# Performance work log

Hardware: AMD Instinct MI355X
Metric: run time of the kernel (lower is better)

The kernel has to match this reference:

```python
import jax, jax.numpy as jnp
import numpy as np

B = 32          # batch size
N = 32          # image dim -> P = N*N points per sample
P = N * N
F = 64          # point feature dim (= MLP output)
K = 32          # max_neighbors
R = 0.1         # ball-query radius
EPS = 1e-5      # batchnorm eps


def setup_inputs() -> dict:
    key = jax.random.key(0)
    ks = jax.random.split(key, 4)
    NP = B * P
    x = jax.random.normal(ks[0], (NP, F), jnp.float32)
    pos = jax.random.uniform(ks[1], (NP, 2), jnp.float32)
    # module requires exactly N*N points per sample, sorted by batch
    batch = jnp.repeat(jnp.arange(B, dtype=jnp.int32), P)
    # MLP([66,128,64]) params: Linear->BN->ReLU->Linear
    W1 = jax.random.normal(ks[2], (F + 2, 128), jnp.float32) * (1.0 / np.sqrt(F + 2))
    b1 = jnp.zeros((128,), jnp.float32)
    gamma1 = jnp.ones((128,), jnp.float32)
    beta1 = jnp.zeros((128,), jnp.float32)
    W2 = jax.random.normal(ks[3], (128, F), jnp.float32) * (1.0 / np.sqrt(128))
    b2 = jnp.zeros((F,), jnp.float32)
    return {"x": x, "pos": pos, "batch": batch, "W1": W1, "b1": b1,
            "gamma1": gamma1, "beta1": beta1, "W2": W2, "b2": b2}


def reference(x, pos, batch, W1, b1, gamma1, beta1, W2, b2):
    NP = x.shape[0]
    posb = pos.reshape(B, P, 2)
    # pixel (target) index of every query point: batch*N*N + row*N + col
    rows = jnp.clip((pos[:, 1] * N).astype(jnp.int32), 0, N - 1)
    cols = jnp.clip((pos[:, 0] * N).astype(jnp.int32), 0, N - 1)
    pix = batch.astype(jnp.int32) * (N * N) + rows * N + cols          # [NP]
    # radius ball query within each batch sample (deterministic: nearest-K within R)
    d2 = jnp.sum((posb[:, :, None, :] - posb[:, None, :, :]) ** 2, -1)  # [B,P,P]
    d2 = jnp.where(d2 <= R * R, d2, jnp.inf)
    negd, nbr = jax.lax.top_k(-d2, K)                                   # [B,P,K]
    valid = jnp.isfinite(negd)
    src = (jnp.arange(B, dtype=jnp.int32)[:, None, None] * P + nbr).reshape(-1)  # [B*P*K]
    dst = jnp.broadcast_to(pix.reshape(B, P)[:, :, None], (B, P, K)).reshape(-1)
    mask = valid.reshape(-1) & (src != dst)          # remove_self_loops
    # PointNetConv message: concat(x_j, pos_j - pos_i); pos_i indexed by mapped target
    relpos = pos[src] - pos[dst]
    msg_nb = jnp.concatenate([x[src], relpos], -1)                    # [B*P*K, F+2]
    # add_self_loops: edge (i, i) for every node -> relpos = 0
    msg_self = jnp.concatenate([x, jnp.zeros_like(pos)], -1)          # [NP, F+2]
    msg = jnp.concatenate([msg_nb, msg_self], 0)
    m = jnp.concatenate([mask, jnp.ones((NP,), bool)], 0)
    tgt = jnp.concatenate([dst, jnp.arange(NP, dtype=jnp.int32)], 0)
    # MLP: Linear -> BatchNorm(training stats over valid messages) -> ReLU -> Linear
    z = msg @ W1 + b1
    mf = m.astype(z.dtype)[:, None]
    cnt = jnp.sum(mf)
    mean = jnp.sum(z * mf, 0, keepdims=True) / cnt
    var = jnp.sum(((z - mean) ** 2) * mf, 0, keepdims=True) / cnt
    h = jax.nn.relu((z - mean) / jnp.sqrt(var + EPS) * gamma1 + beta1)
    o = h @ W2 + b2                                                    # [M, F]
    # scatter-max aggregation into B*N*N pixel nodes (self loops make all nonempty)
    o = jnp.where(m[:, None], o, -jnp.inf)
    pixel_features = jax.ops.segment_max(o, tgt, num_segments=NP)
    images = pixel_features.reshape(B, N, N, F).transpose(0, 3, 1, 2)
    return images
```

## Files before the change

### kernel.cpp

```cpp
#include <hip/hip_runtime.h>
#include <hip/hip_bf16.h>
#include <hip/hip_fp16.h>
#include <math.h>


#define NPTS   32768
#define KNB    32
#define BN_EPS 1e-5f

#define WS_NBRS     0u
#define WS_NBRCNT   4194304u
#define WS_DEG      4325376u
#define WS_STX      4456448u
#define WS_STY      4587520u
#define WS_DEFREP   4718592u
#define WS_SCSH     4719616u
#define WS_W2B      4720640u
#define WS_PART     4737024u
#define WS_Y        5265408u
#define WS_SCRATCH  5265408u
#define WS_WB       13654016u
#define WS_QCNT     22042624u
#define WS_QSTART   22173696u
#define WS_QLIST    22304768u
#define WS_ISLOT    22435840u
#define WS_SELF     22566912u
#define WS_SHP      30955520u
#define WS_BQPART   22566912u

typedef __attribute__((ext_vector_type(8))) _Float16 half8;
typedef __attribute__((ext_vector_type(2))) _Float16 half2v;
typedef __attribute__((ext_vector_type(4))) float floatx4;

__device__ __forceinline__ unsigned short f2h_bits(float f) {
    _Float16 h = (_Float16)f;
    return *reinterpret_cast<unsigned short*>(&h);
}
__device__ __forceinline__ float bf_lo(unsigned int w) { return __uint_as_float(w << 16); }
__device__ __forceinline__ float bf_hi(unsigned int w) { return __uint_as_float(w & 0xffff0000u); }
__device__ __forceinline__ unsigned int pack_bf2(float lo, float hi) {
    __hip_bfloat162 hh = __float22bfloat162_rn(make_float2(lo, hi));
    return *reinterpret_cast<unsigned int*>(&hh);
}
__device__ __forceinline__ unsigned int pack_h2(float lo, float hi) {
    half2v hh = { (_Float16)lo, (_Float16)hi };
    return *reinterpret_cast<unsigned int*>(&hh);
}

__launch_bounds__(256)
__global__ void k_prep(const float* __restrict__ W2, unsigned short* __restrict__ w2b,
                       float* __restrict__ defrep, const float* __restrict__ pos,
                       int* __restrict__ qcnt, int* __restrict__ qstart,
                       int* __restrict__ qlist, int* __restrict__ islot) {
    int tid = threadIdx.x;
    int gt = blockIdx.x * 256 + tid;
    if (gt < 256) defrep[gt] = 0.0f;
    {
        int j  = gt & 7;
        int L  = (gt >> 3) & 63;
        int ks = (gt >> 9) & 3;
        int t4 = gt >> 11;
        int k = ks * 32 + (L >> 4) * 8 + j;
        int n = t4 * 16 + (L & 15);
        w2b[gt] = f2h_bits(W2[k * 64 + n]);
    }
    __shared__ int cntS[1024], preS[1024], offS[1024], pixOf[1024];
    __shared__ int wtot[4];
    int s = blockIdx.x;
    int base = s << 10;
    for (int i = tid; i < 1024; i += 256) cntS[i] = 0;
    __syncthreads();
    for (int ql = tid; ql < 1024; ql += 256) {
        float2 p = *(const float2*)&pos[2 * (base + ql)];
        int row = min(max((int)(p.y * 32.0f), 0), 31);
        int col = min(max((int)(p.x * 32.0f), 0), 31);
        int pixl = row * 32 + col;
        pixOf[ql] = pixl;
        atomicAdd(&cntS[pixl], 1);
    }
    __syncthreads();
    int a0 = cntS[4 * tid], a1 = cntS[4 * tid + 1], a2 = cntS[4 * tid + 2], a3 = cntS[4 * tid + 3];
    int tsum = a0 + a1 + a2 + a3;
    int lane = tid & 63, wv = tid >> 6;
    int v = tsum;
    for (int o = 1; o < 64; o <<= 1) { int u = __shfl_up(v, o); if (lane >= o) v += u; }
    if (lane == 63) wtot[wv] = v;
    __syncthreads();
    int wbase = 0;
    for (int w = 0; w < wv; ++w) wbase += wtot[w];
    int excl = wbase + v - tsum;
    preS[4 * tid] = excl;
    preS[4 * tid + 1] = excl + a0;
    preS[4 * tid + 2] = excl + a0 + a1;
    preS[4 * tid + 3] = excl + a0 + a1 + a2;
    __syncthreads();
    for (int i = tid; i < 1024; i += 256) offS[i] = preS[i];
    __syncthreads();
    for (int ql = tid; ql < 1024; ql += 256) {
        int p = pixOf[ql];
        int slot = atomicAdd(&offS[p], 1);
        qlist[base + slot] = base + ql;
        islot[base + ql] = base + slot;
    }
    for (int i = tid; i < 1024; i += 256) {
        qcnt[base + i] = cntS[i];
        qstart[base + i] = base + preS[i];
    }
}

__launch_bounds__(256)
__global__ void k_ballquery(const float* __restrict__ pos,
                            int* __restrict__ nbrs, int* __restrict__ nbr_cnt,
                            float* __restrict__ bqpart, float* __restrict__ defrep) {
    __shared__ float2 poss[1024];
    __shared__ float accd[1024], accx[1024], accy[1024];
    __shared__ unsigned long long cand[4][256];
    int tid = threadIdx.x, wave = tid >> 6, lane = tid & 63;
    int s = blockIdx.x >> 5;
    int chunk = blockIdx.x & 31;
    int base = s << 10;
    for (int i = tid; i < 1024; i += 256) poss[i] = *(const float2*)&pos[2 * (base + i)];
    for (int i = tid; i < 1024; i += 256) { accd[i] = 0.0f; accx[i] = 0.0f; accy[i] = 0.0f; }
    __syncthreads();
    float2 pr[16];
#pragma unroll
    for (int k = 0; k < 16; ++k) pr[k] = poss[k * 64 + lane];
    unsigned long long lb = (1ull << lane) - 1ull;

    float aD = 0, aE = 0, aF = 0;
    for (int qi = 0; qi < 8; ++qi) {
        int ql = chunk * 32 + wave * 8 + qi;
        int q = base + ql;
        float2 qp = poss[ql];
        int row = min(max((int)(qp.y * 32.0f), 0), 31);
        int col = min(max((int)(qp.x * 32.0f), 0), 31);
        int pixl = row * 32 + col;
        float2 tp = poss[pixl];
        int cnt = 0;
        __builtin_amdgcn_wave_barrier();
#pragma unroll
        for (int k = 0; k < 16; ++k) {
            float dx = pr[k].x - qp.x, dy = pr[k].y - qp.y;
            float d2 = __fadd_rn(__fmul_rn(dx, dx), __fmul_rn(dy, dy));
            bool pred = (d2 <= 0.01f);
            unsigned long long mask = __ballot(pred);
            if (pred) {
                int slot = cnt + (int)__popcll(mask & lb);
                if (slot < 256)
                    cand[wave][slot] = ((unsigned long long)__float_as_uint(d2) << 32)
                                       | (unsigned int)(k * 64 + lane);
            }
            cnt += (int)__popcll(mask);
        }
        cnt = min(cnt, 256);
        __builtin_amdgcn_wave_barrier();
        int osel = 0;
        for (int cb = 0; cb < cnt; cb += 64) {
            int i = cb + lane;
            bool sel = false;
            int j = 0;
            if (i < cnt) {
                unsigned long long key = cand[wave][i];
                j = (int)(key & 0xffffffffu);
                if (cnt <= KNB) {
                    sel = (j != pixl);
                } else {
                    int rank = 0;
                    for (int t = 0; t < cnt; ++t) rank += (cand[wave][t] < key) ? 1 : 0;
                    sel = (rank < KNB) && (j != pixl);
                }
            }
            unsigned long long mask = __ballot(sel);
            if (sel) {
                int slot = osel + (int)__popcll(mask & lb);
                nbrs[q * KNB + slot] = base + j;
                float rx = poss[j].x - tp.x, ry = poss[j].y - tp.y;
                aD += rx * rx; aE += rx * ry; aF += ry * ry;
                atomicAdd(&accd[j], 1.0f);
                atomicAdd(&accx[j], tp.x);
                atomicAdd(&accy[j], tp.y);
            }
            osel += (int)__popcll(mask);
        }
        if (lane == 0) nbr_cnt[q] = osel;
    }
#pragma unroll
    for (int o = 1; o < 64; o <<= 1) {
        aD += __shfl_xor(aD, o); aE += __shfl_xor(aE, o); aF += __shfl_xor(aF, o);
    }
    __syncthreads();
    float* pb = &bqpart[blockIdx.x * 3072];
    for (int i = tid; i < 1024; i += 256) {
        pb[i] = accd[i]; pb[1024 + i] = accx[i]; pb[2048 + i] = accy[i];
    }
    if (tid == 0) {
        int r = (blockIdx.x & 63) * 4;
        atomicAdd(&defrep[r + 0], aD);
        atomicAdd(&defrep[r + 1], aE);
        atomicAdd(&defrep[r + 2], aF);
    }
}

__global__ void k_nodeagg(const float* __restrict__ bqpart, float* __restrict__ deg,
                          float* __restrict__ stx, float* __restrict__ sty) {
    int t = blockIdx.x * 256 + threadIdx.x;
    int s = t >> 10, off = t & 1023;
    const float* pb = &bqpart[(s * 32) * 3072];
    float d = 0, xx = 0, yy = 0;
    for (int j = 0; j < 32; ++j) {
        d  += pb[j * 3072 + off];
        xx += pb[j * 3072 + 1024 + off];
        yy += pb[j * 3072 + 2048 + off];
    }
    deg[t] = d; stx[t] = xx; sty[t] = yy;
}

__launch_bounds__(256)
__global__ void k_y(const float* __restrict__ x, const float* __restrict__ W1,
                    const float* __restrict__ b1, const float* __restrict__ pos,
                    const float* __restrict__ deg, const float* __restrict__ stxA,
                    const float* __restrict__ styA,
                    unsigned int* __restrict__ yb, float* __restrict__ partials) {
    __shared__ float w1s[64 * 128];
    __shared__ float stage[4][512];
    __shared__ float lsum[515];
    int tid = threadIdx.x;
    for (int i = tid; i < 64 * 128; i += 256) w1s[i] = W1[i];
    for (int i = tid; i < 515; i += 256) lsum[i] = 0.0f;
    __syncthreads();
    int wave = tid >> 6, lane = tid & 63;
    int f0 = 2 * lane, f1 = 2 * lane + 1;
    float b10 = b1[f0], b11 = b1[f1];
    float* st = &stage[wave][0];
    float P0 = 0, Q0 = 0, R0 = 0, S0 = 0, P1 = 0, Q1 = 0, R1 = 0, S1 = 0;
    float sB = 0, sC = 0, sDeg = 0;

    for (int it = 0; it < 4; ++it) {
        int nbase = ((blockIdx.x * 4 + wave) * 4 + it) * 8;
        __builtin_amdgcn_wave_barrier();
#pragma unroll
        for (int mm = 0; mm < 8; ++mm)
            st[mm * 64 + lane] = x[(nbase + mm) * 64 + lane];
        __builtin_amdgcn_wave_barrier();
        float z0[8], z1[8];
#pragma unroll
        for (int mm = 0; mm < 8; ++mm) { z0[mm] = b10; z1[mm] = b11; }
        for (int k4 = 0; k4 < 16; ++k4) {
            float2 wv0 = *(const float2*)&w1s[(k4 * 4 + 0) * 128 + f0];
            float2 wv1 = *(const float2*)&w1s[(k4 * 4 + 1) * 128 + f0];
            float2 wv2 = *(const float2*)&w1s[(k4 * 4 + 2) * 128 + f0];
            float2 wv3 = *(const float2*)&w1s[(k4 * 4 + 3) * 128 + f0];
#pragma unroll
            for (int mm = 0; mm < 8; ++mm) {
                float4 mk = *(const float4*)&st[mm * 64 + k4 * 4];
                z0[mm] += mk.x * wv0.x + mk.y * wv1.x + mk.z * wv2.x + mk.w * wv3.x;
                z1[mm] += mk.x * wv0.y + mk.y * wv1.y + mk.z * wv2.y + mk.w * wv3.y;
            }
        }
#pragma unroll
        for (int mm = 0; mm < 8; ++mm) {
            int n = nbase + mm;
            float dg = deg[n];
            float wgt = 1.0f + dg;
            float Bn = dg * pos[2 * n]     - stxA[n];
            float Cn = dg * pos[2 * n + 1] - styA[n];
            float a = z0[mm], bq = z1[mm];
            P0 += wgt * a;  Q0 += wgt * a * a;  R0 += a * Bn;  S0 += a * Cn;
            P1 += wgt * bq; Q1 += wgt * bq * bq; R1 += bq * Bn; S1 += bq * Cn;
            sB += Bn; sC += Cn; sDeg += dg;
            yb[n * 64 + lane] = pack_bf2(a, bq);
        }
    }
    atomicAdd(&lsum[f0], P0);        atomicAdd(&lsum[f1], P1);
    atomicAdd(&lsum[128 + f0], Q0);  atomicAdd(&lsum[128 + f1], Q1);
    atomicAdd(&lsum[256 + f0], R0);  atomicAdd(&lsum[256 + f1], R1);
    atomicAdd(&lsum[384 + f0], S0);  atomicAdd(&lsum[384 + f1], S1);
    if (lane == 0) {
        atomicAdd(&lsum[512], sB);
        atomicAdd(&lsum[513], sC);
        atomicAdd(&lsum[514], sDeg);
    }
    __syncthreads();
    for (int i = tid; i < 515; i += 256) partials[blockIdx.x * 516 + i] = lsum[i];
}

__global__ void k_finalize(const float* __restrict__ gamma, const float* __restrict__ beta,
                           const float* __restrict__ W1, const float* __restrict__ partials,
                           const float* __restrict__ defrep, float* __restrict__ scsh) {
    __shared__ float red[515];
    __shared__ float sDEF[3];
    int tid = threadIdx.x;
    for (int i = tid; i < 515; i += 256) {
        float s = 0;
        for (int b = 0; b < 256; ++b) s += partials[b * 516 + i];
        red[i] = s;
    }
    if (tid < 3) {
        float s = 0;
        for (int r = 0; r < 64; ++r) s += defrep[r * 4 + tid];
        sDEF[tid] = s;
    }
    __syncthreads();
    if (tid < 128) {
        int f = tid;
        float P = red[f], Q = red[128 + f], R = red[256 + f], S = red[384 + f];
        float SB = red[512], SC = red[513], SDeg = red[514];
        float u = W1[8192 + f], v = W1[8320 + f];
        float cntv = 32768.0f + SDeg;
        float mean = (P + u * SB + v * SC) / cntv;
        float E2 = (Q + 2.0f * u * R + 2.0f * v * S
                    + u * u * sDEF[0] + 2.0f * u * v * sDEF[1] + v * v * sDEF[2]) / cntv;
        float var = E2 - mean * mean;
        float sc = gamma[f] / sqrtf(var + BN_EPS);
        scsh[f] = sc;
        scsh[128 + f] = beta[f] - mean * sc;
    }
}

__launch_bounds__(256)
__global__ void k_self(const unsigned int* __restrict__ yb, const float* __restrict__ pos,
                       const float* __restrict__ W1, const float* __restrict__ scsh,
                       const unsigned short* __restrict__ w2b, const float* __restrict__ b2,
                       const int* __restrict__ qcnt,
                       unsigned int* __restrict__ wbuf, unsigned int* __restrict__ shpbuf,
                       float* __restrict__ selfbuf, float* __restrict__ out) {
    __shared__ unsigned short hbuf[4][16 * 136];
    int tid = threadIdx.x, wave = tid >> 6, lane = tid & 63;
    unsigned short* hb = hbuf[wave];
    half8 bfrag[4][4];
#pragma unroll
    for (int t = 0; t < 4; ++t)
#pragma unroll
        for (int ks = 0; ks < 4; ++ks)
            bfrag[t][ks] = *(const half8*)&w2b[((t * 4 + ks) * 64 + lane) * 8];
    int f0 = 2 * lane;
    float sc0 = scsh[f0],     sh0 = scsh[128 + f0];
    float sc1 = scsh[f0 + 1], sh1 = scsh[129 + f0];
    float u0 = W1[8192 + f0], v0 = W1[8320 + f0];
    float u1 = W1[8193 + f0], v1 = W1[8321 + f0];
    float b2v0 = b2[(lane & 15)],      b2v1 = b2[16 + (lane & 15)];
    float b2v2 = b2[32 + (lane & 15)], b2v3 = b2[48 + (lane & 15)];

    int nbase = (blockIdx.x * 4 + wave) * 16;
#pragma unroll
    for (int c = 0; c < 2; ++c) {
        unsigned int yw[8];
#pragma unroll
        for (int j = 0; j < 8; ++j)
            yw[j] = yb[(nbase + c * 8 + j) * 64 + lane];
#pragma unroll
        for (int j = 0; j < 8; ++j) {
            int e = c * 8 + j;
            int nn = nbase + e;
            float y0 = bf_lo(yw[j]), y1 = bf_hi(yw[j]);
            float h0 = fmaxf(y0 * sc0 + sh0, 0.0f);
            float h1 = fmaxf(y1 * sc1 + sh1, 0.0f);
            *(unsigned int*)&hb[e * 136 + f0] = pack_h2(h0, h1);
            float px = pos[2 * nn], py = pos[2 * nn + 1];
            float ts0 = (px * u0 + py * v0) * sc0;
            float ts1 = (px * u1 + py * v1) * sc1;
            wbuf[nn * 64 + lane]   = pack_h2(y0 * sc0 + ts0, y1 * sc1 + ts1);
            shpbuf[nn * 64 + lane] = pack_h2(sh0 - ts0, sh1 - ts1);
        }
    }
    __builtin_amdgcn_wave_barrier();
    floatx4 acc0 = {0,0,0,0}, acc1 = {0,0,0,0}, acc2 = {0,0,0,0}, acc3 = {0,0,0,0};
#pragma unroll
    for (int ks = 0; ks < 4; ++ks) {
        half8 a = *(const half8*)&hb[(lane & 15) * 136 + ks * 32 + (lane >> 4) * 8];
        acc0 = __builtin_amdgcn_mfma_f32_16x16x32_f16(a, bfrag[0][ks], acc0, 0, 0, 0);
        acc1 = __builtin_amdgcn_mfma_f32_16x16x32_f16(a, bfrag[1][ks], acc1, 0, 0, 0);
        acc2 = __builtin_amdgcn_mfma_f32_16x16x32_f16(a, bfrag[2][ks], acc2, 0, 0, 0);
        acc3 = __builtin_amdgcn_mfma_f32_16x16x32_f16(a, bfrag[3][ks], acc3, 0, 0, 0);
    }
    int nrow = nbase + (lane >> 4) * 4;
#pragma unroll
    for (int r = 0; r < 4; ++r) {
        int n = nrow + r;
        float o0 = acc0[r] + b2v0, o1 = acc1[r] + b2v1;
        float o2 = acc2[r] + b2v2, o3 = acc3[r] + b2v3;
        selfbuf[n * 64 + (lane & 15)]      = o0;
        selfbuf[n * 64 + 16 + (lane & 15)] = o1;
        selfbuf[n * 64 + 32 + (lane & 15)] = o2;
        selfbuf[n * 64 + 48 + (lane & 15)] = o3;
        if (qcnt[n] == 0) {
            int obase = (n >> 10) * 65536 + (n & 1023);
            out[obase + ((lane & 15)) * 1024]      = o0;
            out[obase + (16 + (lane & 15)) * 1024] = o1;
            out[obase + (32 + (lane & 15)) * 1024] = o2;
            out[obase + (48 + (lane & 15)) * 1024] = o3;
        }
    }
}

__launch_bounds__(256)
__global__ void k_out(const unsigned int* __restrict__ wbuf,
                      const unsigned int* __restrict__ shpbuf,
                      const float* __restrict__ pos,
                      const unsigned short* __restrict__ w2b, const float* __restrict__ b2,
                      const int* __restrict__ nbrs, const int* __restrict__ nbr_cnt,
                      const int* __restrict__ islot, float* __restrict__ scratch) {
    int tid = threadIdx.x, wave = tid >> 6, lane = tid & 63;
    half8 bfrag[4][4];
#pragma unroll
    for (int t = 0; t < 4; ++t)
#pragma unroll
        for (int ks = 0; ks < 4; ++ks)
            bfrag[t][ks] = *(const half8*)&w2b[((t * 4 + ks) * 64 + lane) * 8];
    float b2l = b2[lane];
    int em = lane & 15;
    int koff = (lane >> 4) * 4;
    int wid = blockIdx.x * 4 + wave;

    for (int qi = 0; qi < 2; ++qi) {
        int q = wid * 2 + qi;
        int m = nbr_cnt[q];
        int b = q >> 10;
        float qx = pos[2 * q], qy = pos[2 * q + 1];
        int row = min(max((int)(qy * 32.0f), 0), 31);
        int col = min(max((int)(qx * 32.0f), 0), 31);
        int pixq = (b << 10) + row * 32 + col;
        uint4 sv0 = *(const uint4*)&shpbuf[pixq * 64 + 0 * 16 + koff];
        uint4 sv1 = *(const uint4*)&shpbuf[pixq * 64 + 1 * 16 + koff];
        uint4 sv2 = *(const uint4*)&shpbuf[pixq * 64 + 2 * 16 + koff];
        uint4 sv3 = *(const uint4*)&shpbuf[pixq * 64 + 3 * 16 + koff];
        int nv = (lane < m) ? nbrs[q * KNB + lane] : 0;
        float om0[4], om1[4], om2[4], om3[4];
#pragma unroll
        for (int r = 0; r < 4; ++r) { om0[r] = -INFINITY; om1[r] = -INFINITY; om2[r] = -INFINITY; om3[r] = -INFINITY; }

        for (int mt = 0; mt * 16 < m; ++mt) {
            int src = __shfl(nv, mt * 16 + em);
            const unsigned int* wp = &wbuf[src * 64 + koff];
            floatx4 a0 = {0,0,0,0}, a1 = {0,0,0,0}, a2 = {0,0,0,0}, a3 = {0,0,0,0};
#pragma unroll
            for (int ks = 0; ks < 4; ++ks) {
                uint4 wv = *(const uint4*)&wp[ks * 16];
                uint4 sv = (ks == 0) ? sv0 : (ks == 1) ? sv1 : (ks == 2) ? sv2 : sv3;
                union { unsigned int u[4]; half8 h8; } af;
#pragma unroll
                for (int qd = 0; qd < 4; ++qd) {
                    unsigned int wd = (qd == 0) ? wv.x : (qd == 1) ? wv.y : (qd == 2) ? wv.z : wv.w;
                    unsigned int sd = (qd == 0) ? sv.x : (qd == 1) ? sv.y : (qd == 2) ? sv.z : sv.w;
                    half2v wh = *reinterpret_cast<half2v*>(&wd);
                    half2v sh = *reinterpret_cast<half2v*>(&sd);
                    half2v zz = { (_Float16)0.0f, (_Float16)0.0f };
                    half2v hh = __builtin_elementwise_max(wh + sh, zz);
                    af.u[qd] = *reinterpret_cast<unsigned int*>(&hh);
                }
                a0 = __builtin_amdgcn_mfma_f32_16x16x32_f16(af.h8, bfrag[0][ks], a0, 0, 0, 0);
                a1 = __builtin_amdgcn_mfma_f32_16x16x32_f16(af.h8, bfrag[1][ks], a1, 0, 0, 0);
                a2 = __builtin_amdgcn_mfma_f32_16x16x32_f16(af.h8, bfrag[2][ks], a2, 0, 0, 0);
                a3 = __builtin_amdgcn_mfma_f32_16x16x32_f16(af.h8, bfrag[3][ks], a3, 0, 0, 0);
            }
            int rowb = (lane >> 4) * 4;
#pragma unroll
            for (int r = 0; r < 4; ++r) {
                int e = mt * 16 + rowb + r;
                if (e < m) {
                    om0[r] = fmaxf(om0[r], a0[r]);
                    om1[r] = fmaxf(om1[r], a1[r]);
                    om2[r] = fmaxf(om2[r], a2[r]);
                    om3[r] = fmaxf(om3[r], a3[r]);
                }
            }
        }
        float w0 = fmaxf(fmaxf(om0[0], om0[1]), fmaxf(om0[2], om0[3]));
        float w1 = fmaxf(fmaxf(om1[0], om1[1]), fmaxf(om1[2], om1[3]));
        float w2 = fmaxf(fmaxf(om2[0], om2[1]), fmaxf(om2[2], om2[3]));
        float w3 = fmaxf(fmaxf(om3[0], om3[1]), fmaxf(om3[2], om3[3]));
        w0 = fmaxf(w0, __shfl_xor(w0, 16)); w0 = fmaxf(w0, __shfl_xor(w0, 32));
        w1 = fmaxf(w1, __shfl_xor(w1, 16)); w1 = fmaxf(w1, __shfl_xor(w1, 32));
        w2 = fmaxf(w2, __shfl_xor(w2, 16)); w2 = fmaxf(w2, __shfl_xor(w2, 32));
        w3 = fmaxf(w3, __shfl_xor(w3, 16)); w3 = fmaxf(w3, __shfl_xor(w3, 32));
        int g4 = lane >> 4;
        float vf = (g4 == 0) ? w0 : (g4 == 1) ? w1 : (g4 == 2) ? w2 : w3;
        vf += b2l;
        scratch[islot[q] * 64 + lane] = vf;
    }
}

__launch_bounds__(256)
__global__ void k_gather(const float* __restrict__ scratch, const float* __restrict__ selfbuf,
                         const int* __restrict__ qcnt, const int* __restrict__ qstart,
                         float* __restrict__ out) {
    int tid = threadIdx.x, wave = tid >> 6, lane = tid & 63;
    int n = blockIdx.x * 4 + wave;
    int c = qcnt[n];
    if (c == 0) return;
    int qs = qstart[n];
    float v = selfbuf[n * 64 + lane];
    for (int i = 0; i < c; ++i)
        v = fmaxf(v, scratch[(qs + i) * 64 + lane]);
    out[(n >> 10) * 65536 + lane * 1024 + (n & 1023)] = v;
}

extern "C" void kernel_launch(void* const* d_in, const int* in_sizes, int n_in,
                              void* d_out, int out_size, void* d_ws, size_t ws_size,
                              hipStream_t stream) {
    const float* x     = (const float*)d_in[0];
    const float* pos   = (const float*)d_in[1];
    const float* W1    = (const float*)d_in[3];
    const float* b1    = (const float*)d_in[4];
    const float* gamma = (const float*)d_in[5];
    const float* beta  = (const float*)d_in[6];
    const float* W2    = (const float*)d_in[7];
    const float* b2    = (const float*)d_in[8];
    float* out = (float*)d_out;
    char* ws = (char*)d_ws;
    int*   nbrs     = (int*)(ws + WS_NBRS);
    int*   nbr_cnt  = (int*)(ws + WS_NBRCNT);
    float* deg      = (float*)(ws + WS_DEG);
    float* stx      = (float*)(ws + WS_STX);
    float* sty      = (float*)(ws + WS_STY);
    float* defrep   = (float*)(ws + WS_DEFREP);
    float* scsh     = (float*)(ws + WS_SCSH);
    unsigned short* w2b = (unsigned short*)(ws + WS_W2B);
    float* partials = (float*)(ws + WS_PART);
    unsigned int* yb = (unsigned int*)(ws + WS_Y);
    float* scratch  = (float*)(ws + WS_SCRATCH);
    unsigned int* wbuf = (unsigned int*)(ws + WS_WB);
    int* qcnt   = (int*)(ws + WS_QCNT);
    int* qstart = (int*)(ws + WS_QSTART);
    int* qlist  = (int*)(ws + WS_QLIST);
    int* islot  = (int*)(ws + WS_ISLOT);
    float* selfbuf = (float*)(ws + WS_SELF);
    unsigned int* shpbuf = (unsigned int*)(ws + WS_SHP);
    float* bqpart   = (float*)(ws + WS_BQPART);

    k_prep<<<32, 256, 0, stream>>>(W2, w2b, defrep, pos, qcnt, qstart, qlist, islot);
    k_ballquery<<<1024, 256, 0, stream>>>(pos, nbrs, nbr_cnt, bqpart, defrep);
    k_nodeagg<<<128, 256, 0, stream>>>(bqpart, deg, stx, sty);
    k_y<<<256, 256, 0, stream>>>(x, W1, b1, pos, deg, stx, sty, yb, partials);
    k_finalize<<<1, 256, 0, stream>>>(gamma, beta, W1, partials, defrep, scsh);
    k_self<<<NPTS / 64, 256, 0, stream>>>(yb, pos, W1, scsh, w2b, b2, qcnt,
                                          wbuf, shpbuf, selfbuf, out);
    k_out<<<NPTS / 8, 256, 0, stream>>>(wbuf, shpbuf, pos, w2b, b2,
                                        nbrs, nbr_cnt, islot, scratch);
    k_gather<<<NPTS / 4, 256, 0, stream>>>(scratch, selfbuf, qcnt, qstart, out);
}
```

Baseline: 247.2 us.

## Merge prep into ball query, fold node aggregation into k_y, unroll k_out

Folds the pixel-map prep work into the ball-query launch by having the first 32 blocks take a separate branch, with a shared-memory union so both roles fit one kernel. The node-degree reduction kernel is removed: k_y now runs 512-thread blocks and reduces the per-block partials into shared memory itself. Per-block deformation sums are written into the partials buffer and summed in finalize, replacing the global atomics and the zero-init. k_out replaces its neighbor-tile loop with two explicit 16-edge tiles whose gathers are all issued up front, which raises register use.

```diff
diff --git a/kernel.cpp b/kernel.cpp
--- a/kernel.cpp
+++ b/kernel.cpp
@@ -10,10 +10,6 @@
 
 #define WS_NBRS     0u
 #define WS_NBRCNT   4194304u
-#define WS_DEG      4325376u
-#define WS_STX      4456448u
-#define WS_STY      4587520u
-#define WS_DEFREP   4718592u
 #define WS_SCSH     4719616u
 #define WS_W2B      4720640u
 #define WS_PART     4737024u
@@ -47,95 +43,105 @@
     return *reinterpret_cast<unsigned int*>(&hh);
 }
 
+union ShBQ {
+    struct {
+        float2 poss[1024];
+        float accd[1024], accx[1024], accy[1024];
+        unsigned long long cand[4][256];
+    } bq;
+    struct {
+        int cntS[1024], preS[1024], offS[1024], pixOf[1024];
+        int wtot[4];
+    } pm;
+};
+
 __launch_bounds__(256)
-__global__ void k_prep(const float* __restrict__ W2, unsigned short* __restrict__ w2b,
-                       float* __restrict__ defrep, const float* __restrict__ pos,
-                       int* __restrict__ qcnt, int* __restrict__ qstart,
-                       int* __restrict__ qlist, int* __restrict__ islot) {
+__global__ void k_bq(const float* __restrict__ pos,
+                     int* __restrict__ nbrs, int* __restrict__ nbr_cnt,
+                     float* __restrict__ bqpart,
+                     const float* __restrict__ W2, unsigned short* __restrict__ w2b,
+                     int* __restrict__ qcnt, int* __restrict__ qstart,
+                     int* __restrict__ qlist, int* __restrict__ islot) {
+    __shared__ ShBQ sh;
     int tid = threadIdx.x;
-    int gt = blockIdx.x * 256 + tid;
-    if (gt < 256) defrep[gt] = 0.0f;
-    {
-        int j  = gt & 7;
-        int L  = (gt >> 3) & 63;
-        int ks = (gt >> 9) & 3;
-        int t4 = gt >> 11;
-        int k = ks * 32 + (L >> 4) * 8 + j;
-        int n = t4 * 16 + (L & 15);
-        w2b[gt] = f2h_bits(W2[k * 64 + n]);
-    }
-    __shared__ int cntS[1024], preS[1024], offS[1024], pixOf[1024];
-    __shared__ int wtot[4];
-    int s = blockIdx.x;
+
+    if (blockIdx.x < 32) {
+        int s = blockIdx.x;
+        int gt = s * 256 + tid;
+        {
+            int j  = gt & 7;
+            int L  = (gt >> 3) & 63;
+            int ks = (gt >> 9) & 3;
+            int t4 = gt >> 11;
+            int k = ks * 32 + (L >> 4) * 8 + j;
+            int n = t4 * 16 + (L & 15);
+            w2b[gt] = f2h_bits(W2[k * 64 + n]);
+        }
+        int base = s << 10;
+        for (int i = tid; i < 1024; i += 256) sh.pm.cntS[i] = 0;
+        __syncthreads();
+        for (int ql = tid; ql < 1024; ql += 256) {
+            float2 p = *(const float2*)&pos[2 * (base + ql)];
+            int row = min(max((int)(p.y * 32.0f), 0), 31);
+            int col = min(max((int)(p.x * 32.0f), 0), 31);
+            int pixl = row * 32 + col;
+            sh.pm.pixOf[ql] = pixl;
+            atomicAdd(&sh.pm.cntS[pixl], 1);
+        }
+        __syncthreads();
+        int a0 = sh.pm.cntS[4 * tid], a1 = sh.pm.cntS[4 * tid + 1];
+        int a2 = sh.pm.cntS[4 * tid + 2], a3 = sh.pm.cntS[4 * tid + 3];
+        int tsum = a0 + a1 + a2 + a3;
+        int lane = tid & 63, wv = tid >> 6;
+        int v = tsum;
+        for (int o = 1; o < 64; o <<= 1) { int u = __shfl_up(v, o); if (lane >= o) v += u; }
+        if (lane == 63) sh.pm.wtot[wv] = v;
+        __syncthreads();
+        int wbase = 0;
+        for (int w = 0; w < wv; ++w) wbase += sh.pm.wtot[w];
+        int excl = wbase + v - tsum;
+        sh.pm.preS[4 * tid] = excl;
+        sh.pm.preS[4 * tid + 1] = excl + a0;
+        sh.pm.preS[4 * tid + 2] = excl + a0 + a1;
+        sh.pm.preS[4 * tid + 3] = excl + a0 + a1 + a2;
+        __syncthreads();
+        for (int i = tid; i < 1024; i += 256) sh.pm.offS[i] = sh.pm.preS[i];
+        __syncthreads();
+        for (int ql = tid; ql < 1024; ql += 256) {
+            int p = sh.pm.pixOf[ql];
+            int slot = atomicAdd(&sh.pm.offS[p], 1);
+            qlist[base + slot] = base + ql;
+            islot[base + ql] = base + slot;
+        }
+        for (int i = tid; i < 1024; i += 256) {
+            qcnt[base + i] = sh.pm.cntS[i];
+            qstart[base + i] = base + sh.pm.preS[i];
+        }
+        return;
+    }
+
+    int bqid = blockIdx.x - 32;
+    int wave = tid >> 6, lane = tid & 63;
+    int s = bqid >> 5;
+    int chunk = bqid & 31;
     int base = s << 10;
-    for (int i = tid; i < 1024; i += 256) cntS[i] = 0;
-    __syncthreads();
-    for (int ql = tid; ql < 1024; ql += 256) {
-        float2 p = *(const float2*)&pos[2 * (base + ql)];
-        int row = min(max((int)(p.y * 32.0f), 0), 31);
-        int col = min(max((int)(p.x * 32.0f), 0), 31);
-        int pixl = row * 32 + col;
-        pixOf[ql] = pixl;
-        atomicAdd(&cntS[pixl], 1);
-    }
-    __syncthreads();
-    int a0 = cntS[4 * tid], a1 = cntS[4 * tid + 1], a2 = cntS[4 * tid + 2], a3 = cntS[4 * tid + 3];
-    int tsum = a0 + a1 + a2 + a3;
-    int lane = tid & 63, wv = tid >> 6;
-    int v = tsum;
-    for (int o = 1; o < 64; o <<= 1) { int u = __shfl_up(v, o); if (lane >= o) v += u; }
-    if (lane == 63) wtot[wv] = v;
-    __syncthreads();
-    int wbase = 0;
-    for (int w = 0; w < wv; ++w) wbase += wtot[w];
-    int excl = wbase + v - tsum;
-    preS[4 * tid] = excl;
-    preS[4 * tid + 1] = excl + a0;
-    preS[4 * tid + 2] = excl + a0 + a1;
-    preS[4 * tid + 3] = excl + a0 + a1 + a2;
-    __syncthreads();
-    for (int i = tid; i < 1024; i += 256) offS[i] = preS[i];
-    __syncthreads();
-    for (int ql = tid; ql < 1024; ql += 256) {
-        int p = pixOf[ql];
-        int slot = atomicAdd(&offS[p], 1);
-        qlist[base + slot] = base + ql;
-        islot[base + ql] = base + slot;
-    }
-    for (int i = tid; i < 1024; i += 256) {
-        qcnt[base + i] = cntS[i];
-        qstart[base + i] = base + preS[i];
-    }
-}
-
-__launch_bounds__(256)
-__global__ void k_ballquery(const float* __restrict__ pos,
-                            int* __restrict__ nbrs, int* __restrict__ nbr_cnt,
-                            float* __restrict__ bqpart, float* __restrict__ defrep) {
-    __shared__ float2 poss[1024];
-    __shared__ float accd[1024], accx[1024], accy[1024];
-    __shared__ unsigned long long cand[4][256];
-    int tid = threadIdx.x, wave = tid >> 6, lane = tid & 63;
-    int s = blockIdx.x >> 5;
-    int chunk = blockIdx.x & 31;
-    int base = s << 10;
-    for (int i = tid; i < 1024; i += 256) poss[i] = *(const float2*)&pos[2 * (base + i)];
-    for (int i = tid; i < 1024; i += 256) { accd[i] = 0.0f; accx[i] = 0.0f; accy[i] = 0.0f; }
+    for (int i = tid; i < 1024; i += 256) sh.bq.poss[i] = *(const float2*)&pos[2 * (base + i)];
+    for (int i = tid; i < 1024; i += 256) { sh.bq.accd[i] = 0.0f; sh.bq.accx[i] = 0.0f; sh.bq.accy[i] = 0.0f; }
     __syncthreads();
     float2 pr[16];
 #pragma unroll
-    for (int k = 0; k < 16; ++k) pr[k] = poss[k * 64 + lane];
+    for (int k = 0; k < 16; ++k) pr[k] = sh.bq.poss[k * 64 + lane];
     unsigned long long lb = (1ull << lane) - 1ull;
 
     float aD = 0, aE = 0, aF = 0;
     for (int qi = 0; qi < 8; ++qi) {
         int ql = chunk * 32 + wave * 8 + qi;
         int q = base + ql;
-        float2 qp = poss[ql];
+        float2 qp = sh.bq.poss[ql];
         int row = min(max((int)(qp.y * 32.0f), 0), 31);
         int col = min(max((int)(qp.x * 32.0f), 0), 31);
         int pixl = row * 32 + col;
-        float2 tp = poss[pixl];
+        float2 tp = sh.bq.poss[pixl];
         int cnt = 0;
         __builtin_amdgcn_wave_barrier();
 #pragma unroll
@@ -147,8 +153,8 @@
             if (pred) {
                 int slot = cnt + (int)__popcll(mask & lb);
                 if (slot < 256)
-                    cand[wave][slot] = ((unsigned long long)__float_as_uint(d2) << 32)
-                                       | (unsigned int)(k * 64 + lane);
+                    sh.bq.cand[wave][slot] = ((unsigned long long)__float_as_uint(d2) << 32)
+                                             | (unsigned int)(k * 64 + lane);
             }
             cnt += (int)__popcll(mask);
         }
@@ -160,13 +166,13 @@
             bool sel = false;
             int j = 0;
             if (i < cnt) {
-                unsigned long long key = cand[wave][i];
+                unsigned long long key = sh.bq.cand[wave][i];
                 j = (int)(key & 0xffffffffu);
                 if (cnt <= KNB) {
                     sel = (j != pixl);
                 } else {
                     int rank = 0;
-                    for (int t = 0; t < cnt; ++t) rank += (cand[wave][t] < key) ? 1 : 0;
+                    for (int t = 0; t < cnt; ++t) rank += (sh.bq.cand[wave][t] < key) ? 1 : 0;
                     sel = (rank < KNB) && (j != pixl);
                 }
             }
@@ -174,11 +180,11 @@
             if (sel) {
                 int slot = osel + (int)__popcll(mask & lb);
                 nbrs[q * KNB + slot] = base + j;
-                float rx = poss[j].x - tp.x, ry = poss[j].y - tp.y;
+                float rx = sh.bq.poss[j].x - tp.x, ry = sh.bq.poss[j].y - tp.y;
                 aD += rx * rx; aE += rx * ry; aF += ry * ry;
-                atomicAdd(&accd[j], 1.0f);
-                atomicAdd(&accx[j], tp.x);
-                atomicAdd(&accy[j], tp.y);
+                atomicAdd(&sh.bq.accd[j], 1.0f);
+                atomicAdd(&sh.bq.accx[j], tp.x);
+                atomicAdd(&sh.bq.accy[j], tp.y);
             }
             osel += (int)__popcll(mask);
         }
@@ -189,44 +195,38 @@
         aD += __shfl_xor(aD, o); aE += __shfl_xor(aE, o); aF += __shfl_xor(aF, o);
     }
     __syncthreads();
-    float* pb = &bqpart[blockIdx.x * 3072];
+    float* pb = &bqpart[bqid * 3076];
     for (int i = tid; i < 1024; i += 256) {
-        pb[i] = accd[i]; pb[1024 + i] = accx[i]; pb[2048 + i] = accy[i];
-    }
-    if (tid == 0) {
-        int r = (blockIdx.x & 63) * 4;
-        atomicAdd(&defrep[r + 0], aD);
-        atomicAdd(&defrep[r + 1], aE);
-        atomicAdd(&defrep[r + 2], aF);
-    }
-}
-
-__global__ void k_nodeagg(const float* __restrict__ bqpart, float* __restrict__ deg,
-                          float* __restrict__ stx, float* __restrict__ sty) {
-    int t = blockIdx.x * 256 + threadIdx.x;
-    int s = t >> 10, off = t & 1023;
-    const float* pb = &bqpart[(s * 32) * 3072];
-    float d = 0, xx = 0, yy = 0;
-    for (int j = 0; j < 32; ++j) {
-        d  += pb[j * 3072 + off];
-        xx += pb[j * 3072 + 1024 + off];
-        yy += pb[j * 3072 + 2048 + off];
-    }
-    deg[t] = d; stx[t] = xx; sty[t] = yy;
-}
-
-__launch_bounds__(256)
+        pb[i] = sh.bq.accd[i]; pb[1024 + i] = sh.bq.accx[i]; pb[2048 + i] = sh.bq.accy[i];
+    }
+    if (tid == 0) { pb[3072] = aD; pb[3073] = aE; pb[3074] = aF; }
+}
+
+__launch_bounds__(512)
 __global__ void k_y(const float* __restrict__ x, const float* __restrict__ W1,
                     const float* __restrict__ b1, const float* __restrict__ pos,
-                    const float* __restrict__ deg, const float* __restrict__ stxA,
-                    const float* __restrict__ styA,
+                    const float* __restrict__ bqpart,
                     unsigned int* __restrict__ yb, float* __restrict__ partials) {
     __shared__ float w1s[64 * 128];
-    __shared__ float stage[4][512];
+    __shared__ float stage[8][512];
     __shared__ float lsum[515];
+    __shared__ float degS[128], stxS[128], styS[128];
     int tid = threadIdx.x;
-    for (int i = tid; i < 64 * 128; i += 256) w1s[i] = W1[i];
-    for (int i = tid; i < 515; i += 256) lsum[i] = 0.0f;
+    int nblock = blockIdx.x * 128;
+    for (int i = tid; i < 64 * 128; i += 512) w1s[i] = W1[i];
+    for (int i = tid; i < 515; i += 512) lsum[i] = 0.0f;
+    if (tid < 128) {
+        int n = nblock + tid;
+        int s = n >> 10, off = n & 1023;
+        const float* pb = &bqpart[(s * 32) * 3076];
+        float d = 0, xx = 0, yy = 0;
+        for (int j = 0; j < 32; ++j) {
+            d  += pb[j * 3076 + off];
+            xx += pb[j * 3076 + 1024 + off];
+            yy += pb[j * 3076 + 2048 + off];
+        }
+        degS[tid] = d; stxS[tid] = xx; styS[tid] = yy;
+    }
     __syncthreads();
     int wave = tid >> 6, lane = tid & 63;
     int f0 = 2 * lane, f1 = 2 * lane + 1;
@@ -235,8 +235,8 @@
     float P0 = 0, Q0 = 0, R0 = 0, S0 = 0, P1 = 0, Q1 = 0, R1 = 0, S1 = 0;
     float sB = 0, sC = 0, sDeg = 0;
 
-    for (int it = 0; it < 4; ++it) {
-        int nbase = ((blockIdx.x * 4 + wave) * 4 + it) * 8;
+    for (int it = 0; it < 2; ++it) {
+        int nbase = nblock + (wave * 2 + it) * 8;
         __builtin_amdgcn_wave_barrier();
 #pragma unroll
         for (int mm = 0; mm < 8; ++mm)
@@ -260,16 +260,18 @@
 #pragma unroll
         for (int mm = 0; mm < 8; ++mm) {
             int n = nbase + mm;
-            float dg = deg[n];
+            int li = n - nblock;
+            float dg = degS[li];
             float wgt = 1.0f + dg;
-            float Bn = dg * pos[2 * n]     - stxA[n];
-            float Cn = dg * pos[2 * n + 1] - styA[n];
+            float Bn = dg * pos[2 * n]     - stxS[li];
+            float Cn = dg * pos[2 * n + 1] - styS[li];
             float a = z0[mm], bq = z1[mm];
             P0 += wgt * a;  Q0 += wgt * a * a;  R0 += a * Bn;  S0 += a * Cn;
             P1 += wgt * bq; Q1 += wgt * bq * bq; R1 += bq * Bn; S1 += bq * Cn;
             sB += Bn; sC += Cn; sDeg += dg;
             yb[n * 64 + lane] = pack_bf2(a, bq);
         }
+        __builtin_amdgcn_wave_barrier();
     }
     atomicAdd(&lsum[f0], P0);        atomicAdd(&lsum[f1], P1);
     atomicAdd(&lsum[128 + f0], Q0);  atomicAdd(&lsum[128 + f1], Q1);
@@ -281,24 +283,29 @@
         atomicAdd(&lsum[514], sDeg);
     }
     __syncthreads();
-    for (int i = tid; i < 515; i += 256) partials[blockIdx.x * 516 + i] = lsum[i];
+    for (int i = tid; i < 515; i += 512) partials[blockIdx.x * 516 + i] = lsum[i];
 }
 
 __global__ void k_finalize(const float* __restrict__ gamma, const float* __restrict__ beta,
                            const float* __restrict__ W1, const float* __restrict__ partials,
-                           const float* __restrict__ defrep, float* __restrict__ scsh) {
+                           const float* __restrict__ bqpart, float* __restrict__ scsh) {
     __shared__ float red[515];
     __shared__ float sDEF[3];
     int tid = threadIdx.x;
+    if (tid < 3) sDEF[tid] = 0.0f;
     for (int i = tid; i < 515; i += 256) {
         float s = 0;
         for (int b = 0; b < 256; ++b) s += partials[b * 516 + i];
         red[i] = s;
     }
-    if (tid < 3) {
-        float s = 0;
-        for (int r = 0; r < 64; ++r) s += defrep[r * 4 + tid];
-        sDEF[tid] = s;
+    __syncthreads();
+    {
+        float td = 0, te = 0, tf = 0;
+        for (int b = tid; b < 1024; b += 256) {
+            const float* pb = &bqpart[b * 3076 + 3072];
+            td += pb[0]; te += pb[1]; tf += pb[2];
+        }
+        atomicAdd(&sDEF[0], td); atomicAdd(&sDEF[1], te); atomicAdd(&sDEF[2], tf);
     }
     __syncthreads();
     if (tid < 128) {
@@ -416,52 +423,92 @@
         int q = wid * 2 + qi;
         int m = nbr_cnt[q];
         int b = q >> 10;
+        float om0[4], om1[4], om2[4], om3[4];
+#pragma unroll
+        for (int r = 0; r < 4; ++r) { om0[r] = -INFINITY; om1[r] = -INFINITY; om2[r] = -INFINITY; om3[r] = -INFINITY; }
         float qx = pos[2 * q], qy = pos[2 * q + 1];
         int row = min(max((int)(qy * 32.0f), 0), 31);
         int col = min(max((int)(qx * 32.0f), 0), 31);
         int pixq = (b << 10) + row * 32 + col;
-        uint4 sv0 = *(const uint4*)&shpbuf[pixq * 64 + 0 * 16 + koff];
-        uint4 sv1 = *(const uint4*)&shpbuf[pixq * 64 + 1 * 16 + koff];
-        uint4 sv2 = *(const uint4*)&shpbuf[pixq * 64 + 2 * 16 + koff];
-        uint4 sv3 = *(const uint4*)&shpbuf[pixq * 64 + 3 * 16 + koff];
-        int nv = (lane < m) ? nbrs[q * KNB + lane] : 0;
-        float om0[4], om1[4], om2[4], om3[4];
-#pragma unroll
-        for (int r = 0; r < 4; ++r) { om0[r] = -INFINITY; om1[r] = -INFINITY; om2[r] = -INFINITY; om3[r] = -INFINITY; }
-
-        for (int mt = 0; mt * 16 < m; ++mt) {
-            int src = __shfl(nv, mt * 16 + em);
-            const unsigned int* wp = &wbuf[src * 64 + koff];
-            floatx4 a0 = {0,0,0,0}, a1 = {0,0,0,0}, a2 = {0,0,0,0}, a3 = {0,0,0,0};
-#pragma unroll
-            for (int ks = 0; ks < 4; ++ks) {
-                uint4 wv = *(const uint4*)&wp[ks * 16];
-                uint4 sv = (ks == 0) ? sv0 : (ks == 1) ? sv1 : (ks == 2) ? sv2 : sv3;
-                union { unsigned int u[4]; half8 h8; } af;
-#pragma unroll
-                for (int qd = 0; qd < 4; ++qd) {
-                    unsigned int wd = (qd == 0) ? wv.x : (qd == 1) ? wv.y : (qd == 2) ? wv.z : wv.w;
-                    unsigned int sd = (qd == 0) ? sv.x : (qd == 1) ? sv.y : (qd == 2) ? sv.z : sv.w;
-                    half2v wh = *reinterpret_cast<half2v*>(&wd);
-                    half2v sh = *reinterpret_cast<half2v*>(&sd);
-                    half2v zz = { (_Float16)0.0f, (_Float16)0.0f };
-                    half2v hh = __builtin_elementwise_max(wh + sh, zz);
-                    af.u[qd] = *reinterpret_cast<unsigned int*>(&hh);
+
+        if (m > 0) {
+            uint4 sv[4];
+#pragma unroll
+            for (int ks = 0; ks < 4; ++ks)
+                sv[ks] = *(const uint4*)&shpbuf[pixq * 64 + ks * 16 + koff];
+            int nv = (lane < m) ? nbrs[q * KNB + lane] : 0;
+            int src0 = __shfl(nv, em);
+            int src1 = __shfl(nv, 16 + em);
+            bool two = (m > 16);
+            uint4 g0[4], g1[4];
+            const unsigned int* wp0 = &wbuf[src0 * 64 + koff];
+#pragma unroll
+            for (int ks = 0; ks < 4; ++ks) g0[ks] = *(const uint4*)&wp0[ks * 16];
+            if (two) {
+                const unsigned int* wp1 = &wbuf[src1 * 64 + koff];
+#pragma unroll
+                for (int ks = 0; ks < 4; ++ks) g1[ks] = *(const uint4*)&wp1[ks * 16];
+            }
+            int rowb = (lane >> 4) * 4;
+            {
+                floatx4 a0 = {0,0,0,0}, a1 = {0,0,0,0}, a2 = {0,0,0,0}, a3 = {0,0,0,0};
+#pragma unroll
+                for (int ks = 0; ks < 4; ++ks) {
+                    union { unsigned int u[4]; half8 h8; } af;
+#pragma unroll
+                    for (int qd = 0; qd < 4; ++qd) {
+                        unsigned int wd = (qd == 0) ? g0[ks].x : (qd == 1) ? g0[ks].y : (qd == 2) ? g0[ks].z : g0[ks].w;
+                        unsigned int sd = (qd == 0) ? sv[ks].x : (qd == 1) ? sv[ks].y : (qd == 2) ? sv[ks].z : sv[ks].w;
+                        half2v wh = *reinterpret_cast<half2v*>(&wd);
+                        half2v shh = *reinterpret_cast<half2v*>(&sd);
+                        half2v zz = { (_Float16)0.0f, (_Float16)0.0f };
+                        half2v hh = __builtin_elementwise_max(wh + shh, zz);
+                        af.u[qd] = *reinterpret_cast<unsigned int*>(&hh);
+                    }
+                    a0 = __builtin_amdgcn_mfma_f32_16x16x32_f16(af.h8, bfrag[0][ks], a0, 0, 0, 0);
+                    a1 = __builtin_amdgcn_mfma_f32_16x16x32_f16(af.h8, bfrag[1][ks], a1, 0, 0, 0);
+                    a2 = __builtin_amdgcn_mfma_f32_16x16x32_f16(af.h8, bfrag[2][ks], a2, 0, 0, 0);
+                    a3 = __builtin_amdgcn_mfma_f32_16x16x32_f16(af.h8, bfrag[3][ks], a3, 0, 0, 0);
                 }
-                a0 = __builtin_amdgcn_mfma_f32_16x16x32_f16(af.h8, bfrag[0][ks], a0, 0, 0, 0);
-                a1 = __builtin_amdgcn_mfma_f32_16x16x32_f16(af.h8, bfrag[1][ks], a1, 0, 0, 0);
-                a2 = __builtin_amdgcn_mfma_f32_16x16x32_f16(af.h8, bfrag[2][ks], a2, 0, 0, 0);
-                a3 = __builtin_amdgcn_mfma_f32_16x16x32_f16(af.h8, bfrag[3][ks], a3, 0, 0, 0);
-            }
-            int rowb = (lane >> 4) * 4;
-#pragma unroll
-            for (int r = 0; r < 4; ++r) {
-                int e = mt * 16 + rowb + r;
-                if (e < m) {
-                    om0[r] = fmaxf(om0[r], a0[r]);
-                    om1[r] = fmaxf(om1[r], a1[r]);
-                    om2[r] = fmaxf(om2[r], a2[r]);
-                    om3[r] = fmaxf(om3[r], a3[r]);
+#pragma unroll
+                for (int r = 0; r < 4; ++r) {
+                    if (rowb + r < m) {
+                        om0[r] = fmaxf(om0[r], a0[r]);
+                        om1[r] = fmaxf(om1[r], a1[r]);
+                        om2[r] = fmaxf(om2[r], a2[r]);
+                        om3[r] = fmaxf(om3[r], a3[r]);
+                    }
+                }
+            }
+            if (two) {
+                floatx4 a0 = {0,0,0,0}, a1 = {0,0,0,0}, a2 = {0,0,0,0}, a3 = {0,0,0,0};
+#pragma unroll
+                for (int ks = 0; ks < 4; ++ks) {
+                    union { unsigned int u[4]; half8 h8; } af;
+#pragma unroll
+                    for (int qd = 0; qd < 4; ++qd) {
+                        unsigned int wd = (qd == 0) ? g1[ks].x : (qd == 1) ? g1[ks].y : (qd == 2) ? g1[ks].z : g1[ks].w;
+                        unsigned int sd = (qd == 0) ? sv[ks].x : (qd == 1) ? sv[ks].y : (qd == 2) ? sv[ks].z : sv[ks].w;
+                        half2v wh = *reinterpret_cast<half2v*>(&wd);
+                        half2v shh = *reinterpret_cast<half2v*>(&sd);
+                        half2v zz = { (_Float16)0.0f, (_Float16)0.0f };
+                        half2v hh = __builtin_elementwise_max(wh + shh, zz);
+                        af.u[qd] = *reinterpret_cast<unsigned int*>(&hh);
+                    }
+                    a0 = __builtin_amdgcn_mfma_f32_16x16x32_f16(af.h8, bfrag[0][ks], a0, 0, 0, 0);
+                    a1 = __builtin_amdgcn_mfma_f32_16x16x32_f16(af.h8, bfrag[1][ks], a1, 0, 0, 0);
+                    a2 = __builtin_amdgcn_mfma_f32_16x16x32_f16(af.h8, bfrag[2][ks], a2, 0, 0, 0);
+                    a3 = __builtin_amdgcn_mfma_f32_16x16x32_f16(af.h8, bfrag[3][ks], a3, 0, 0, 0);
+                }
+#pragma unroll
+                for (int r = 0; r < 4; ++r) {
+                    int e = 16 + rowb + r;
+                    if (e < m) {
+                        om0[r] = fmaxf(om0[r], a0[r]);
+                        om1[r] = fmaxf(om1[r], a1[r]);
+                        om2[r] = fmaxf(om2[r], a2[r]);
+                        om3[r] = fmaxf(om3[r], a3[r]);
+                    }
                 }
             }
         }
@@ -510,10 +557,6 @@
     char* ws = (char*)d_ws;
     int*   nbrs     = (int*)(ws + WS_NBRS);
     int*   nbr_cnt  = (int*)(ws + WS_NBRCNT);
-    float* deg      = (float*)(ws + WS_DEG);
-    float* stx      = (float*)(ws + WS_STX);
-    float* sty      = (float*)(ws + WS_STY);
-    float* defrep   = (float*)(ws + WS_DEFREP);
     float* scsh     = (float*)(ws + WS_SCSH);
     unsigned short* w2b = (unsigned short*)(ws + WS_W2B);
     float* partials = (float*)(ws + WS_PART);
@@ -528,11 +571,10 @@
     unsigned int* shpbuf = (unsigned int*)(ws + WS_SHP);
     float* bqpart   = (float*)(ws + WS_BQPART);
 
-    k_prep<<<32, 256, 0, stream>>>(W2, w2b, defrep, pos, qcnt, qstart, qlist, islot);
-    k_ballquery<<<1024, 256, 0, stream>>>(pos, nbrs, nbr_cnt, bqpart, defrep);
-    k_nodeagg<<<128, 256, 0, stream>>>(bqpart, deg, stx, sty);
-    k_y<<<256, 256, 0, stream>>>(x, W1, b1, pos, deg, stx, sty, yb, partials);
-    k_finalize<<<1, 256, 0, stream>>>(gamma, beta, W1, partials, defrep, scsh);
+    k_bq<<<1056, 256, 0, stream>>>(pos, nbrs, nbr_cnt, bqpart, W2, w2b,
+                                   qcnt, qstart, qlist, islot);
+    k_y<<<256, 512, 0, stream>>>(x, W1, b1, pos, bqpart, yb, partials);
+    k_finalize<<<1, 256, 0, stream>>>(gamma, beta, W1, partials, bqpart, scsh);
     k_self<<<NPTS / 64, 256, 0, stream>>>(yb, pos, W1, scsh, w2b, b2, qcnt,
                                           wbuf, shpbuf, selfbuf, out);
     k_out<<<NPTS / 8, 256, 0, stream>>>(wbuf, shpbuf, pos, w2b, b2,
```

Result: no change. 246.0 us (-0.5%).
